# Optimization experiments

Hardware: AMD Instinct MI355X
Metric: run time of the kernel (lower is better)

## Reference

```python
import jax, jax.numpy as jnp
import numpy as np

OUT, IN, GS = 11008, 4096, 128   # out_features, in_features, group_size
G = IN // GS                     # num_groups = 32 (in_features divisible by group_size)
TOKENS = 8192                    # batch 4 * seq 2048


def setup_inputs() -> dict:
    key = jax.random.key(0)
    k1, k2, k3, k4, k5 = jax.random.split(key, 5)
    x = jax.random.normal(k1, (TOKENS, IN), dtype=jnp.float32)
    # packed int4 weights: two nibbles per byte, stored as int32 in [0,256)
    qweight = jax.random.randint(k2, (OUT, IN // 2), 0, 256, dtype=jnp.int32)
    # realistic GPTQ scales (small positive) and zero-points in [0,15]
    scales = jax.random.uniform(k3, (OUT, G), dtype=jnp.float32) * 0.01 + 1e-3
    zeros = jax.random.uniform(k4, (OUT, G), dtype=jnp.float32) * 15.0
    bias = jax.random.normal(k5, (OUT,), dtype=jnp.float32) * 0.01
    return {"x": x, "qweight": qweight, "scales": scales, "zeros": zeros, "bias": bias}


def _dequant(qweight, scales, zeros):
    # unpack: column 2i = low nibble, column 2i+1 = high nibble (matches torch loop)
    low = (qweight & 15).astype(jnp.float32)          # [OUT, IN/2]
    high = ((qweight >> 4) & 15).astype(jnp.float32)  # [OUT, IN/2]
    w = jnp.stack([low, high], axis=-1).reshape(OUT, IN)
    # group-wise dequant: (q - zero) * scale per group of GS input channels
    w = (w.reshape(OUT, G, GS) - zeros[:, :, None]) * scales[:, :, None]
    return w.reshape(OUT, IN)


def reference(x, qweight, scales, zeros, bias):
    w = _dequant(qweight, scales, zeros)   # [OUT, IN] fp32
    # F.linear: x @ w.T + bias
    return jnp.einsum('ti,oi->to', x, w) + bias
```

## Files before the change

### kernel.cpp

```cpp
#include <hip/hip_runtime.h>
#include <stdint.h>

#define OUTF 11008
#define INF  4096
#define NG   32
#define TOK  8192
#define KB4  2048

#define BM 256
#define BN 256
#define BK 64
#define NT (INF / BK)
#define GX (OUTF / BN)
#define GY (TOK / BM)
#define NWG (GX * GY)

typedef unsigned short u16;
typedef __attribute__((ext_vector_type(8))) short bf16x8;
typedef __attribute__((ext_vector_type(4))) float f32x4;

__device__ inline u16 f2bf(float f) {
  union { float f; uint32_t u; } v; v.f = f;
  return (u16)((v.u + 0x7fff + ((v.u >> 16) & 1)) >> 16);
}

__device__ inline void async_copy16(const void* g, const void* l) {
  __builtin_amdgcn_global_load_lds(
      (__attribute__((address_space(1))) void*)(g),
      (__attribute__((address_space(3))) void*)(l), 16, 0, 0);
}

#define FENCE() asm volatile("" ::: "memory")
#define BAR()   do { FENCE(); __builtin_amdgcn_s_barrier(); FENCE(); } while (0)
#define VMCNT(n) asm volatile("s_waitcnt vmcnt(" #n ")" ::: "memory")


#define NXU ((long long)TOK * INF / 4)
#define NWU ((long long)OUTF * KB4 / 4)
#define PREPBLK 2048

__global__ __launch_bounds__(256) void prep(const float* __restrict__ X,
                                            const int* __restrict__ QW,
                                            const float* __restrict__ scales,
                                            const float* __restrict__ zeros,
                                            u16* __restrict__ Xb,
                                            u16* __restrict__ Wb) {
  const long long stride = (long long)gridDim.x * 256;
  for (long long i = (long long)blockIdx.x * 256 + threadIdx.x; i < NXU + NWU;
       i += stride) {
    if (i < NXU) {
      const float4 f = ((const float4*)X)[i];
      union { u16 t[4]; uint2 v; } u;
      u.t[0] = f2bf(f.x); u.t[1] = f2bf(f.y);
      u.t[2] = f2bf(f.z); u.t[3] = f2bf(f.w);
      ((uint2*)Xb)[i] = u.v;
    } else {
      const long long j = i - NXU;
      const int o = (int)(j >> 9);
      const int c0 = ((int)j & 511) * 4;
      const int g = c0 >> 6;
      const float s = scales[o * NG + g];
      const float zs = -zeros[o * NG + g] * s;
      const int4 q = ((const int4*)QW)[j];
      const int qq[4] = {q.x, q.y, q.z, q.w};
      union { u16 t[8]; int4 v; } u;
#pragma unroll
      for (int k = 0; k < 4; ++k) {
        u.t[2 * k]     = f2bf(fmaf((float)(qq[k] & 15), s, zs));
        u.t[2 * k + 1] = f2bf(fmaf((float)((qq[k] >> 4) & 15), s, zs));
      }
      ((int4*)Wb)[j] = u.v;
    }
  }
}


__global__ __launch_bounds__(512, 2) void gemm_pre512(const u16* __restrict__ A,
                                                      const u16* __restrict__ B,
                                                      const float* __restrict__ bias,
                                                      float* __restrict__ C) {
  __shared__ __align__(16) u16 As[2][BM * BK];
  __shared__ __align__(16) u16 Bs[2][BN * BK];
  const int tid = threadIdx.x;
  const int lane = tid & 63;
  const int wid = __builtin_amdgcn_readfirstlane(tid >> 6);

  const int lin = blockIdx.x;
  const int wg = (lin & 7) * (NWG / 8) + (lin >> 3);
  const int bm = wg / GX;
  const int bn = wg % GX;

  const u16* Ab = A + (size_t)bm * BM * INF;
  const u16* Bb = B + (size_t)bn * BN * INF;

  const int rowoff = tid >> 3;
  const int gran = (tid & 7) ^ (rowoff & 7);
  const u16* Asrc = Ab + (size_t)rowoff * INF + gran * 8;
  const u16* Bsrc = Bb + (size_t)rowoff * INF + gran * 8;
  const int wid8 = wid * 8;

  const int rr = lane & 15;
  const int q4 = lane >> 4;
  const int wm = wid >> 2;
  const int wn = wid & 3;

  f32x4 acc[8][4] = {};
  bf16x8 bq[4];

#define STAGE1(LDS, SRC, TT, R0)                                               \
  async_copy16((SRC) + (size_t)(R0) * INF + (size_t)(TT) * BK,                 \
               (const char*)(LDS) + ((R0) + wid8) * 128);

#define RD_A4(DST, S, KS, MH)                                                  \
  _Pragma("unroll") for (int mi = 0; mi < 4; ++mi)                             \
    DST[mi] = *(const bf16x8*)&As[S][                                          \
        (wm * 128 + (MH) * 64 + mi * 16 + rr) * BK +                           \
        ((((KS) * 4 + q4) ^ (rr & 7)) * 8)];

#define RD_B4(DST, S, KS)                                                      \
  _Pragma("unroll") for (int ni = 0; ni < 4; ++ni)                             \
    DST[ni] = *(const bf16x8*)&Bs[S][                                          \
        (wn * 64 + ni * 16 + rr) * BK +                                        \
        ((((KS) * 4 + q4) ^ (rr & 7)) * 8)];

#define MFMA16(RA, RB, MH)                                                     \
  do {                                                                         \
    __builtin_amdgcn_s_setprio(1);                                             \
    _Pragma("unroll") for (int mi = 0; mi < 4; ++mi)                           \
      _Pragma("unroll") for (int ni = 0; ni < 4; ++ni)                         \
        acc[(MH) * 4 + mi][ni] = __builtin_amdgcn_mfma_f32_16x16x32_bf16(      \
            RA[mi], RB[ni], acc[(MH) * 4 + mi][ni], 0, 0, 0);                  \
    __builtin_amdgcn_s_setprio(0);                                             \
  } while (0)

  STAGE1(&As[0][0], Asrc, 0, 0)   STAGE1(&As[0][0], Asrc, 0, 128)
  STAGE1(&As[0][0], Asrc, 0, 64)  STAGE1(&As[0][0], Asrc, 0, 192)
  STAGE1(&Bs[0][0], Bsrc, 0, 0)   STAGE1(&Bs[0][0], Bsrc, 0, 64)
  STAGE1(&Bs[0][0], Bsrc, 0, 128) STAGE1(&Bs[0][0], Bsrc, 0, 192)
  STAGE1(&As[1][0], Asrc, 1, 0)   STAGE1(&As[1][0], Asrc, 1, 128)
  VMCNT(2);
  BAR();

  for (int t = 0; t < NT; t += 2) {
    {
      bf16x8 ra[4];
      RD_A4(ra, 0, 0, 0) RD_B4(bq, 0, 0)
      STAGE1(&Bs[1][0], Bsrc, t + 1, 0) STAGE1(&Bs[1][0], Bsrc, t + 1, 64)
      BAR(); MFMA16(ra, bq, 0); BAR();
    }
    {
      bf16x8 ra[4];
      RD_A4(ra, 0, 0, 1)
      STAGE1(&Bs[1][0], Bsrc, t + 1, 128) STAGE1(&Bs[1][0], Bsrc, t + 1, 192)
      BAR(); MFMA16(ra, bq, 1); BAR();
    }
    {
      bf16x8 ra[4];
      RD_A4(ra, 0, 1, 0) RD_B4(bq, 0, 1)
      STAGE1(&As[1][0], Asrc, t + 1, 64) STAGE1(&As[1][0], Asrc, t + 1, 192)
      BAR(); MFMA16(ra, bq, 0); BAR();
    }
    {
      bf16x8 ra[4];
      RD_A4(ra, 0, 1, 1)
      if (t + 2 < NT) {
        STAGE1(&As[0][0], Asrc, t + 2, 0) STAGE1(&As[0][0], Asrc, t + 2, 128)
        VMCNT(2);
      } else {
        VMCNT(0);
      }
      BAR(); MFMA16(ra, bq, 1); BAR();
    }
    {
      bf16x8 ra[4];
      RD_A4(ra, 1, 0, 0) RD_B4(bq, 1, 0)
      if (t + 2 < NT) {
        STAGE1(&Bs[0][0], Bsrc, t + 2, 0) STAGE1(&Bs[0][0], Bsrc, t + 2, 64)
      }
      BAR(); MFMA16(ra, bq, 0); BAR();
    }
    {
      bf16x8 ra[4];
      RD_A4(ra, 1, 0, 1)
      if (t + 2 < NT) {
        STAGE1(&Bs[0][0], Bsrc, t + 2, 128) STAGE1(&Bs[0][0], Bsrc, t + 2, 192)
      }
      BAR(); MFMA16(ra, bq, 1); BAR();
    }
    {
      bf16x8 ra[4];
      RD_A4(ra, 1, 1, 0) RD_B4(bq, 1, 1)
      if (t + 2 < NT) {
        STAGE1(&As[0][0], Asrc, t + 2, 64) STAGE1(&As[0][0], Asrc, t + 2, 192)
      }
      BAR(); MFMA16(ra, bq, 0); BAR();
    }
    {
      bf16x8 ra[4];
      RD_A4(ra, 1, 1, 1)
      if (t + 3 < NT) {
        STAGE1(&As[1][0], Asrc, t + 3, 0) STAGE1(&As[1][0], Asrc, t + 3, 128)
        VMCNT(2);
      } else {
        VMCNT(0);
      }
      BAR(); MFMA16(ra, bq, 1); BAR();
    }
  }

  const int ncol = lane & 15;
  const int qrow = (lane >> 4) * 4;
  float bv[4];
#pragma unroll
  for (int ni = 0; ni < 4; ++ni)
    bv[ni] = bias[bn * BN + wn * 64 + ni * 16 + ncol];
#pragma unroll
  for (int mi = 0; mi < 8; ++mi)
#pragma unroll
    for (int ni = 0; ni < 4; ++ni) {
      const int gn = bn * BN + wn * 64 + ni * 16 + ncol;
#pragma unroll
      for (int r = 0; r < 4; ++r) {
        const int gm = bm * BM + wm * 128 + mi * 16 + qrow + r;
        C[(size_t)gm * OUTF + gn] = acc[mi][ni][r] + bv[ni];
      }
    }
}


#define FBM 128
#define FBN 128

#define FMFMA_COMPUTE()                                                       \
  do {                                                                        \
    const int frr = lane & 15;                                                \
    const int fq4 = lane >> 4;                                                \
    _Pragma("unroll") for (int ks = 0; ks < 2; ++ks) {                        \
      bf16x8 fa[4], fb[4];                                                    \
      const int kk = (((ks * 4 + fq4) ^ (frr & 7)) * 8);                      \
      _Pragma("unroll") for (int i = 0; i < 4; ++i) {                         \
        fa[i] = *(const bf16x8*)&Asf[(mwave + i * 16 + frr) * BK + kk];       \
        fb[i] = *(const bf16x8*)&Bsf[(nwave + i * 16 + frr) * BK + kk];       \
      }                                                                       \
      _Pragma("unroll") for (int mi = 0; mi < 4; ++mi)                        \
        _Pragma("unroll") for (int ni = 0; ni < 4; ++ni)                      \
          facc[mi][ni] = __builtin_amdgcn_mfma_f32_16x16x32_bf16(             \
              fa[mi], fb[ni], facc[mi][ni], 0, 0, 0);                         \
    }                                                                         \
  } while (0)

__global__ __launch_bounds__(256) void gemm_fused(const float* __restrict__ X,
                                                  const int* __restrict__ QW,
                                                  const float* __restrict__ scales,
                                                  const float* __restrict__ zeros,
                                                  const float* __restrict__ bias,
                                                  float* __restrict__ C) {
  __shared__ __align__(16) u16 Asf[FBM * BK];
  __shared__ __align__(16) u16 Bsf[FBN * BK];
  const int tid = threadIdx.x;
  const int lane = tid & 63;
  const int wid = tid >> 6;
  const int bm = blockIdx.y, bn = blockIdx.x;
  const int row = tid >> 1;
  const int half = tid & 1;
  const float* xr = X + (size_t)(bm * FBM + row) * INF + half * 32;
  const int* qr = QW + (size_t)(bn * FBN + row) * KB4 + half * 16;
  const float* srow = scales + (size_t)(bn * FBN + row) * NG;
  const float* zrow = zeros + (size_t)(bn * FBN + row) * NG;
  const int mwave = (wid >> 1) * 64;
  const int nwave = (wid & 1) * 64;
  f32x4 facc[4][4] = {};

  for (int kb = 0; kb < INF / BK; ++kb) {
    const int k0 = kb * BK;
    union { u16 t[32]; int4 v[4]; } ta, tb;
#pragma unroll
    for (int j = 0; j < 8; ++j) {
      const float4 f = *(const float4*)(xr + k0 + j * 4);
      ta.t[4 * j]     = f2bf(f.x);
      ta.t[4 * j + 1] = f2bf(f.y);
      ta.t[4 * j + 2] = f2bf(f.z);
      ta.t[4 * j + 3] = f2bf(f.w);
    }
    {
      const float s = srow[kb >> 1];
      const float zs = -zrow[kb >> 1] * s;
#pragma unroll
      for (int j = 0; j < 4; ++j) {
        const int4 q = *(const int4*)(qr + kb * 32 + j * 4);
        const int qq[4] = {q.x, q.y, q.z, q.w};
#pragma unroll
        for (int u = 0; u < 4; ++u) {
          tb.t[8 * j + 2 * u]     = f2bf(fmaf((float)(qq[u] & 15), s, zs));
          tb.t[8 * j + 2 * u + 1] = f2bf(fmaf((float)((qq[u] >> 4) & 15), s, zs));
        }
      }
    }
    __syncthreads();
#pragma unroll
    for (int j = 0; j < 4; ++j) {
      *(int4*)&Asf[row * BK + (((half * 4 + j) ^ (row & 7)) * 8)] = ta.v[j];
      *(int4*)&Bsf[row * BK + (((half * 4 + j) ^ (row & 7)) * 8)] = tb.v[j];
    }
    __syncthreads();
    FMFMA_COMPUTE();
  }
  {
    const int ncol = lane & 15;
    const int qrow = (lane >> 4) * 4;
#pragma unroll
    for (int mi = 0; mi < 4; ++mi)
#pragma unroll
      for (int ni = 0; ni < 4; ++ni) {
        const int gn = bn * FBN + nwave + ni * 16 + ncol;
        const float bvv = bias[gn];
#pragma unroll
        for (int r = 0; r < 4; ++r) {
          const int gm = bm * FBM + mwave + mi * 16 + qrow + r;
          C[(size_t)gm * OUTF + gn] = facc[mi][ni][r] + bvv;
        }
      }
  }
}


extern "C" void kernel_launch(void* const* d_in, const int* in_sizes, int n_in,
                              void* d_out, int out_size, void* d_ws, size_t ws_size,
                              hipStream_t stream) {
  const float* x = (const float*)d_in[0];
  const int* qw = (const int*)d_in[1];
  const float* scales = (const float*)d_in[2];
  const float* zeros = (const float*)d_in[3];
  const float* bias = (const float*)d_in[4];
  float* out = (float*)d_out;

  const size_t needW = (size_t)OUTF * INF * sizeof(u16);
  const size_t needX = (size_t)TOK * INF * sizeof(u16);

  if (ws_size >= needW + needX) {
    u16* Wb = (u16*)d_ws;
    u16* Xb = (u16*)((char*)d_ws + needW);
    prep<<<PREPBLK, 256, 0, stream>>>(x, qw, scales, zeros, Xb, Wb);
    gemm_pre512<<<dim3(NWG), 512, 0, stream>>>(Xb, Wb, bias, out);
  } else {
    gemm_fused<<<dim3(OUTF / FBN, TOK / FBM), 256, 0, stream>>>(x, qw, scales, zeros, bias, out);
  }
}
```

Baseline: 1.296 ms.

## Reschedule GEMM prefetch order, remap tiles per XCD, use nontemporal loads/stores

Reorders the async global-to-LDS staging in the main GEMM loop so B and A sub-tiles are prefetched further ahead, with deeper vmcnt waits placed after the MFMA block instead of before. Replaces the workgroup-to-tile mapping with an XCD-aware scheme that gives each XCD a contiguous set of M tiles and groups of 8 N tiles, aiming at better L2 reuse. Also uses nontemporal loads in the prep kernel and nontemporal stores for the output to reduce cache pollution. The new staging order carries a risk of LDS read/write hazards if the wait counts are wrong.

```diff
diff --git a/kernel.cpp b/kernel.cpp
--- a/kernel.cpp
+++ b/kernel.cpp
@@ -18,6 +18,7 @@
 typedef unsigned short u16;
 typedef __attribute__((ext_vector_type(8))) short bf16x8;
 typedef __attribute__((ext_vector_type(4))) float f32x4;
+typedef __attribute__((ext_vector_type(4))) int i32x4;
 
 __device__ inline u16 f2bf(float f) {
   union { float f; uint32_t u; } v; v.f = f;
@@ -49,10 +50,10 @@
   for (long long i = (long long)blockIdx.x * 256 + threadIdx.x; i < NXU + NWU;
        i += stride) {
     if (i < NXU) {
-      const float4 f = ((const float4*)X)[i];
+      const f32x4 f = __builtin_nontemporal_load((const f32x4*)X + i);
       union { u16 t[4]; uint2 v; } u;
-      u.t[0] = f2bf(f.x); u.t[1] = f2bf(f.y);
-      u.t[2] = f2bf(f.z); u.t[3] = f2bf(f.w);
+      u.t[0] = f2bf(f[0]); u.t[1] = f2bf(f[1]);
+      u.t[2] = f2bf(f[2]); u.t[3] = f2bf(f[3]);
       ((uint2*)Xb)[i] = u.v;
     } else {
       const long long j = i - NXU;
@@ -61,13 +62,12 @@
       const int g = c0 >> 6;
       const float s = scales[o * NG + g];
       const float zs = -zeros[o * NG + g] * s;
-      const int4 q = ((const int4*)QW)[j];
-      const int qq[4] = {q.x, q.y, q.z, q.w};
+      const i32x4 q = __builtin_nontemporal_load((const i32x4*)QW + j);
       union { u16 t[8]; int4 v; } u;
 #pragma unroll
       for (int k = 0; k < 4; ++k) {
-        u.t[2 * k]     = f2bf(fmaf((float)(qq[k] & 15), s, zs));
-        u.t[2 * k + 1] = f2bf(fmaf((float)((qq[k] >> 4) & 15), s, zs));
+        u.t[2 * k]     = f2bf(fmaf((float)(q[k] & 15), s, zs));
+        u.t[2 * k + 1] = f2bf(fmaf((float)((q[k] >> 4) & 15), s, zs));
       }
       ((int4*)Wb)[j] = u.v;
     }
@@ -86,9 +86,19 @@
   const int wid = __builtin_amdgcn_readfirstlane(tid >> 6);
 
   const int lin = blockIdx.x;
-  const int wg = (lin & 7) * (NWG / 8) + (lin >> 3);
-  const int bm = wg / GX;
-  const int bn = wg % GX;
+  const int xcd = lin & 7;
+  const int wgc = lin >> 3;
+  int bmr, bn;
+  if (wgc < 160) {
+    const int g = wgc >> 5, r = wgc & 31;
+    bn = g * 8 + (r & 7);
+    bmr = r >> 3;
+  } else {
+    const int r = wgc - 160;
+    bn = 40 + r % 3;
+    bmr = r / 3;
+  }
+  const int bm = xcd * 4 + bmr;
 
   const u16* Ab = A + (size_t)bm * BM * INF;
   const u16* Bb = B + (size_t)bn * BN * INF;
@@ -134,24 +144,26 @@
   } while (0)
 
   STAGE1(&As[0][0], Asrc, 0, 0)   STAGE1(&As[0][0], Asrc, 0, 128)
-  STAGE1(&As[0][0], Asrc, 0, 64)  STAGE1(&As[0][0], Asrc, 0, 192)
   STAGE1(&Bs[0][0], Bsrc, 0, 0)   STAGE1(&Bs[0][0], Bsrc, 0, 64)
   STAGE1(&Bs[0][0], Bsrc, 0, 128) STAGE1(&Bs[0][0], Bsrc, 0, 192)
-  STAGE1(&As[1][0], Asrc, 1, 0)   STAGE1(&As[1][0], Asrc, 1, 128)
-  VMCNT(2);
+  STAGE1(&As[0][0], Asrc, 0, 64)  STAGE1(&As[0][0], Asrc, 0, 192)
+  STAGE1(&Bs[1][0], Bsrc, 1, 0)   STAGE1(&Bs[1][0], Bsrc, 1, 64)
+  VMCNT(4);
   BAR();
 
   for (int t = 0; t < NT; t += 2) {
     {
       bf16x8 ra[4];
       RD_A4(ra, 0, 0, 0) RD_B4(bq, 0, 0)
-      STAGE1(&Bs[1][0], Bsrc, t + 1, 0) STAGE1(&Bs[1][0], Bsrc, t + 1, 64)
-      BAR(); MFMA16(ra, bq, 0); BAR();
+      STAGE1(&Bs[1][0], Bsrc, t + 1, 128) STAGE1(&Bs[1][0], Bsrc, t + 1, 192)
+      BAR(); MFMA16(ra, bq, 0);
+      VMCNT(4);
+      BAR();
     }
     {
       bf16x8 ra[4];
       RD_A4(ra, 0, 0, 1)
-      STAGE1(&Bs[1][0], Bsrc, t + 1, 128) STAGE1(&Bs[1][0], Bsrc, t + 1, 192)
+      STAGE1(&As[1][0], Asrc, t + 1, 0) STAGE1(&As[1][0], Asrc, t + 1, 128)
       BAR(); MFMA16(ra, bq, 1); BAR();
     }
     {
@@ -163,48 +175,38 @@
     {
       bf16x8 ra[4];
       RD_A4(ra, 0, 1, 1)
-      if (t + 2 < NT) {
-        STAGE1(&As[0][0], Asrc, t + 2, 0) STAGE1(&As[0][0], Asrc, t + 2, 128)
-        VMCNT(2);
-      } else {
-        VMCNT(0);
-      }
+      if (t + 2 < NT) { STAGE1(&Bs[0][0], Bsrc, t + 2, 0) STAGE1(&Bs[0][0], Bsrc, t + 2, 64) }
+      BAR(); MFMA16(ra, bq, 1);
+      if (t + 2 < NT) { VMCNT(4); } else { VMCNT(0); }
+      BAR();
+    }
+    {
+      bf16x8 ra[4];
+      RD_A4(ra, 1, 0, 0) RD_B4(bq, 1, 0)
+      if (t + 2 < NT) { STAGE1(&Bs[0][0], Bsrc, t + 2, 128) STAGE1(&Bs[0][0], Bsrc, t + 2, 192) }
+      BAR(); MFMA16(ra, bq, 0);
+      if (t + 2 < NT) { VMCNT(4); } else { VMCNT(0); }
+      BAR();
+    }
+    {
+      bf16x8 ra[4];
+      RD_A4(ra, 1, 0, 1)
+      if (t + 2 < NT) { STAGE1(&As[0][0], Asrc, t + 2, 0) STAGE1(&As[0][0], Asrc, t + 2, 128) }
       BAR(); MFMA16(ra, bq, 1); BAR();
     }
     {
       bf16x8 ra[4];
-      RD_A4(ra, 1, 0, 0) RD_B4(bq, 1, 0)
-      if (t + 2 < NT) {
-        STAGE1(&Bs[0][0], Bsrc, t + 2, 0) STAGE1(&Bs[0][0], Bsrc, t + 2, 64)
-      }
+      RD_A4(ra, 1, 1, 0) RD_B4(bq, 1, 1)
+      if (t + 2 < NT) { STAGE1(&As[0][0], Asrc, t + 2, 64) STAGE1(&As[0][0], Asrc, t + 2, 192) }
       BAR(); MFMA16(ra, bq, 0); BAR();
     }
     {
       bf16x8 ra[4];
-      RD_A4(ra, 1, 0, 1)
-      if (t + 2 < NT) {
-        STAGE1(&Bs[0][0], Bsrc, t + 2, 128) STAGE1(&Bs[0][0], Bsrc, t + 2, 192)
-      }
-      BAR(); MFMA16(ra, bq, 1); BAR();
-    }
-    {
-      bf16x8 ra[4];
-      RD_A4(ra, 1, 1, 0) RD_B4(bq, 1, 1)
-      if (t + 2 < NT) {
-        STAGE1(&As[0][0], Asrc, t + 2, 64) STAGE1(&As[0][0], Asrc, t + 2, 192)
-      }
-      BAR(); MFMA16(ra, bq, 0); BAR();
-    }
-    {
-      bf16x8 ra[4];
       RD_A4(ra, 1, 1, 1)
-      if (t + 3 < NT) {
-        STAGE1(&As[1][0], Asrc, t + 3, 0) STAGE1(&As[1][0], Asrc, t + 3, 128)
-        VMCNT(2);
-      } else {
-        VMCNT(0);
-      }
-      BAR(); MFMA16(ra, bq, 1); BAR();
+      if (t + 2 < NT) { STAGE1(&Bs[1][0], Bsrc, t + 3, 0) STAGE1(&Bs[1][0], Bsrc, t + 3, 64) }
+      BAR(); MFMA16(ra, bq, 1);
+      if (t + 2 < NT) { VMCNT(4); } else { VMCNT(0); }
+      BAR();
     }
   }
 
@@ -222,7 +224,8 @@
 #pragma unroll
       for (int r = 0; r < 4; ++r) {
         const int gm = bm * BM + wm * 128 + mi * 16 + qrow + r;
-        C[(size_t)gm * OUTF + gn] = acc[mi][ni][r] + bv[ni];
+        __builtin_nontemporal_store(acc[mi][ni][r] + bv[ni],
+                                    &C[(size_t)gm * OUTF + gn]);
       }
     }
 }
```

New measurement: 1.102 ms. 15.0% less time.
